# Kernel optimization log

Hardware: AMD Instinct MI355X
Metric: run time of the kernel (lower is better)

Reference implementation:

```python
import jax, jax.numpy as jnp
import numpy as np

NUM_USERS = 1_000_000
DIM = 64
BATCH = 16384


def setup_inputs() -> dict:
    key = jax.random.key(0)
    k1, k2 = jax.random.split(key)
    x = jax.random.randint(k1, (BATCH,), 0, NUM_USERS, dtype=jnp.int64 if jax.config.jax_enable_x64 else jnp.int32)
    # nn.Linear(num_users, dim).weight has shape [dim, num_users], init std=0.01
    W = jax.random.normal(k2, (DIM, NUM_USERS), dtype=jnp.float32) * 0.01
    return {"x": x, "W": W}


def reference(x, W):
    # one_hot(x, num_users) @ W.T  ==  gather of columns of W, transposed
    # -> [batch, dim]
    return jnp.take(W, x, axis=1).T
```

## Files before the change

kernel.cpp:

```cpp
#include <hip/hip_runtime.h>


#define NUM_USERS 1000000
#define DIM 64
#define BATCH 16384

__global__ __launch_bounds__(256) void UserEmbedding_61873298866785_kernel(
    const int* __restrict__ x,
    const float* __restrict__ W,
    float* __restrict__ out) {
    const int tid = blockIdx.x * blockDim.x + threadIdx.x;
    const int b = tid >> 6;
    const int d = tid & 63;
    const int u = x[b];
    out[tid] = W[(size_t)d * NUM_USERS + (size_t)u];
}

extern "C" void kernel_launch(void* const* d_in, const int* in_sizes, int n_in,
                              void* d_out, int out_size, void* d_ws, size_t ws_size,
                              hipStream_t stream) {
    const int* x = (const int*)d_in[0];
    const float* W = (const float*)d_in[1];
    float* out = (float*)d_out;

    const int total = BATCH * DIM;
    const int block = 256;
    const int grid = total / block;
    UserEmbedding_61873298866785_kernel<<<grid, block, 0, stream>>>(x, W, out);
}
```

Measured before the change: 26.31 us.

## Bucket-sort indices by user id before gathering columns through a shared-memory transpose

Adds a single-block counting sort that groups the batch indices into buckets by user id, writing (user, batch) pairs to workspace. A second kernel gathers W columns for 64 sorted indices per block, so neighbouring lanes read nearby addresses within each W row. It then transposes through shared memory so each output row is written contiguously. The single-block sort runs serially ahead of the gather and adds a second launch, which may outweigh the locality gained from sorting random indices spread over a million columns.

New measurement: 37.74 us. +43.4%, slower.

```diff
diff --git a/kernel.cpp b/kernel.cpp
--- a/kernel.cpp
+++ b/kernel.cpp
@@ -5,15 +5,87 @@
 #define DIM 64
 #define BATCH 16384
 
-__global__ __launch_bounds__(256) void UserEmbedding_61873298866785_kernel(
-    const int* __restrict__ x,
-    const float* __restrict__ W,
+#define NB 4096
+#define SORT_THREADS 1024
+#define EPT (BATCH / SORT_THREADS)
+#define BPT (NB / SORT_THREADS)
+
+#define GBLK 64
+#define GTHREADS 512
+
+__global__ __launch_bounds__(SORT_THREADS) void UE_sort_kernel(
+    const int* __restrict__ x, uint2* __restrict__ pairs) {
+    __shared__ unsigned hist[NB];
+    __shared__ unsigned bases[NB];
+    __shared__ unsigned ssum[SORT_THREADS];
+    const int t = threadIdx.x;
+
+    for (int i = t; i < NB; i += SORT_THREADS) hist[i] = 0u;
+    __syncthreads();
+
+    int u[EPT];
+#pragma unroll
+    for (int i = 0; i < EPT; ++i) {
+        u[i] = x[i * SORT_THREADS + t];
+        atomicAdd(&hist[u[i] >> 8], 1u);
+    }
+    __syncthreads();
+
+    unsigned loc[BPT], s = 0;
+#pragma unroll
+    for (int k = 0; k < BPT; ++k) { loc[k] = hist[t * BPT + k]; s += loc[k]; }
+    ssum[t] = s;
+    __syncthreads();
+    for (int off = 1; off < SORT_THREADS; off <<= 1) {
+        unsigned v = ssum[t];
+        unsigned w = (t >= off) ? ssum[t - off] : 0u;
+        __syncthreads();
+        ssum[t] = v + w;
+        __syncthreads();
+    }
+    unsigned base = ssum[t] - s;
+#pragma unroll
+    for (int k = 0; k < BPT; ++k) { bases[t * BPT + k] = base; base += loc[k]; }
+    __syncthreads();
+
+    for (int i = t; i < NB; i += SORT_THREADS) hist[i] = 0u;
+    __syncthreads();
+
+#pragma unroll
+    for (int i = 0; i < EPT; ++i) {
+        const int uu = u[i];
+        const int bkt = uu >> 8;
+        const unsigned pos = bases[bkt] + atomicAdd(&hist[bkt], 1u);
+        pairs[pos] = make_uint2((unsigned)uu, (unsigned)(i * SORT_THREADS + t));
+    }
+}
+
+__global__ __launch_bounds__(GTHREADS) void UE_gather_kernel(
+    const uint2* __restrict__ pairs, const float* __restrict__ W,
     float* __restrict__ out) {
-    const int tid = blockIdx.x * blockDim.x + threadIdx.x;
-    const int b = tid >> 6;
-    const int d = tid & 63;
-    const int u = x[b];
-    out[tid] = W[(size_t)d * NUM_USERS + (size_t)u];
+    __shared__ float tile[GBLK][DIM + 1];
+    __shared__ unsigned brow[GBLK];
+    const int t = threadIdx.x;
+    const int lane = t & 63;
+    const int w = t >> 6;
+    const int p0 = blockIdx.x * GBLK;
+
+    const uint2 pr = pairs[p0 + lane];
+    if (t < GBLK) brow[t] = pr.y;
+    const size_t u = (size_t)pr.x;
+
+#pragma unroll
+    for (int i = 0; i < DIM / 8; ++i) {
+        const int d = w * 8 + i;
+        tile[lane][d] = W[(size_t)d * NUM_USERS + u];
+    }
+    __syncthreads();
+
+#pragma unroll
+    for (int i = 0; i < DIM / 8; ++i) {
+        const int p = w * 8 + i;
+        out[(size_t)brow[p] * DIM + lane] = tile[p][lane];
+    }
 }
 
 extern "C" void kernel_launch(void* const* d_in, const int* in_sizes, int n_in,
@@ -22,9 +94,8 @@
     const int* x = (const int*)d_in[0];
     const float* W = (const float*)d_in[1];
     float* out = (float*)d_out;
+    uint2* pairs = (uint2*)d_ws;
 
-    const int total = BATCH * DIM;
-    const int block = 256;
-    const int grid = total / block;
-    UserEmbedding_61873298866785_kernel<<<grid, block, 0, stream>>>(x, W, out);
+    UE_sort_kernel<<<1, SORT_THREADS, 0, stream>>>(x, pairs);
+    UE_gather_kernel<<<BATCH / GBLK, GTHREADS, 0, stream>>>(pairs, W, out);
 }
```
